# Kernel tuning notes

Measured on AMD Instinct MI355X. Metric: run time of the kernel, lower is better.

Reference implementation:

```python
import jax, jax.numpy as jnp
import numpy as np


def _perm_mats():
    E = np.zeros((36, 9), np.float32)
    D = np.zeros((9, 36), np.float32)
    c = 0
    for i in range(8):
        for j in range(i + 1, 9):
            E[c, i] = 1.0
            E[c, j] = 1.0
            D[i, c] = 1.0
            D[j, c] = 1.0
            c += 1
    assert c == 36
    return E, D


def setup_inputs() -> dict:
    key = jax.random.key(0)
    B = 32768
    # binary candidate mask: [B, 9 digits, 9 rows, 9 cols]
    mask = jnp.round(jax.random.uniform(key, (B, 9, 9, 9), dtype=jnp.float32))
    E, D = _perm_mats()
    return {"mask": mask, "enc": jnp.asarray(E), "dec": jnp.asarray(D)}


def _nn_compare(x, v):
    # NNCompare: triangular bump == 1 exactly when x == v (for integer-valued x)
    return jnp.minimum(jax.nn.relu(x - (v - 1.0)), jax.nn.relu((v + 1.0) - x))


def _nn_and(x, y):
    return jnp.clip(jnp.minimum(x, y), 0.0, 1.0)


def reference(mask, enc, dec):
    B = mask.shape[0]
    # encode_permutations: 1x1 conv 9 -> 36 (pair selection)
    perms = jnp.einsum('oc,bchw->bohw', enc, mask)          # [B,36,9,9]
    perms = _nn_compare(perms, 2.0)                          # cell contains exactly this pair
    # sum_all_permutations: 1x1 conv 36 -> 1, then == 1
    sum_p = _nn_compare(jnp.sum(perms, axis=1, keepdims=True), 1.0)  # [B,1,9,9]
    perms = _nn_and(perms, sum_p)                            # broadcast over 36 channels
    # box downsample: grouped 3x3 stride-3 sum conv
    down = perms.reshape(B, 36, 3, 3, 3, 3).sum(axis=(3, 5))  # [B,36,3,3]
    down = _nn_compare(down, 2.0)                              # exactly two such cells in box
    up = jnp.repeat(jnp.repeat(down, 3, axis=2), 3, axis=3)    # [B,36,9,9]
    up = _nn_and(up, 1.0 - perms)                              # other cells in the box
    # decode_permutations: 1x1 conv 36 -> 9
    erase = jnp.einsum('oc,bchw->bohw', dec, up)               # [B,9,9,9]
    return _nn_and(mask, 1.0 - erase)
```

## Files before the change

### kernel.cpp

```cpp
#include <hip/hip_runtime.h>
#include <stdint.h>


#define NB 16
#define ELEMS (NB * 729)
#define NWORDS (ELEMS / 4)
#define NBOX (NB * 9)

__global__ __launch_bounds__(256) void sudoku_naked_pair_kernel(
    const float* __restrict__ mask, float* __restrict__ out) {
  __shared__ uint32_t lds32[NWORDS];
  uint8_t* lds8 = (uint8_t*)lds32;

  const int tid = threadIdx.x;
  const size_t base = (size_t)blockIdx.x * ELEMS;

  const float4* in4 = (const float4*)(mask + base);
  for (int i = tid; i < NWORDS; i += 256) {
    float4 v = in4[i];
    lds32[i] = (uint32_t)(v.x != 0.0f)
             | ((uint32_t)(v.y != 0.0f) << 8)
             | ((uint32_t)(v.z != 0.0f) << 16)
             | ((uint32_t)(v.w != 0.0f) << 24);
  }
  __syncthreads();

  if (tid < NBOX) {
    const int b = tid / 9, bi = tid - b * 9;
    const int boxbase = b * 729 + (bi / 3) * 27 + (bi % 3) * 3;

    uint32_t cellm[9] = {0, 0, 0, 0, 0, 0, 0, 0, 0};
#pragma unroll
    for (int d = 0; d < 9; ++d) {
      const uint8_t* p = lds8 + boxbase + d * 81;
#pragma unroll
      for (int r = 0; r < 3; ++r)
#pragma unroll
        for (int c = 0; c < 3; ++c)
          cellm[r * 3 + c] |= ((uint32_t)p[r * 9 + c] & 1u) << d;
    }

    uint32_t pairm[9];
#pragma unroll
    for (int j = 0; j < 9; ++j)
      pairm[j] = (__popc(cellm[j]) == 2) ? cellm[j] : 0u;

    bool naked[9];
#pragma unroll
    for (int j = 0; j < 9; ++j) {
      int cnt = 0;
#pragma unroll
      for (int k = 0; k < 9; ++k) cnt += (pairm[k] == pairm[j]);
      naked[j] = (pairm[j] != 0u) && (cnt == 2);
    }

#pragma unroll
    for (int j = 0; j < 9; ++j) {
      uint32_t er = 0;
#pragma unroll
      for (int k = 0; k < 9; ++k)
        if (naked[k] && pairm[k] != pairm[j]) er |= pairm[k];
      cellm[j] &= ~er;
    }

#pragma unroll
    for (int d = 0; d < 9; ++d) {
      uint8_t* p = lds8 + boxbase + d * 81;
#pragma unroll
      for (int r = 0; r < 3; ++r)
#pragma unroll
        for (int c = 0; c < 3; ++c)
          p[r * 9 + c] = (uint8_t)((cellm[r * 3 + c] >> d) & 1u);
    }
  }
  __syncthreads();

  float4* out4 = (float4*)(out + base);
  for (int i = tid; i < NWORDS; i += 256) {
    uint32_t w = lds32[i];
    float4 v;
    v.x = (float)(w & 0xFFu);
    v.y = (float)((w >> 8) & 0xFFu);
    v.z = (float)((w >> 16) & 0xFFu);
    v.w = (float)(w >> 24);
    out4[i] = v;
  }
}

extern "C" void kernel_launch(void* const* d_in, const int* in_sizes, int n_in,
                              void* d_out, int out_size, void* d_ws, size_t ws_size,
                              hipStream_t stream) {
  const float* mask = (const float*)d_in[0];
  float* out = (float*)d_out;
  const int B = in_sizes[0] / 729;
  const int grid = B / NB;
  sudoku_naked_pair_kernel<<<grid, 256, 0, stream>>>(mask, out);
}
```

Measured before the change: 183.5 us.

## Replace LDS-staged block kernel with one-thread-per-box direct global access

Removes the shared-memory staging and the two barriers. Each thread now loads its box's 81 candidate floats straight from global memory, computes naked-pair eliminations in registers, and writes results directly. This aims to raise occupancy and remove idle threads and LDS traffic. In exchange, global accesses become small strided scalar reads and writes that coalesce poorly, and register pressure rises.

```diff
diff --git a/kernel.cpp b/kernel.cpp
--- a/kernel.cpp
+++ b/kernel.cpp
@@ -2,89 +2,64 @@
 #include <stdint.h>
 
 
-#define NB 16
-#define ELEMS (NB * 729)
-#define NWORDS (ELEMS / 4)
-#define NBOX (NB * 9)
+__global__ __launch_bounds__(256) void sudoku_box_kernel(
+    const float* __restrict__ mask, float* __restrict__ out) {
+  const int t = blockIdx.x * 256 + threadIdx.x;
+  const int board = t / 9;
+  const int bi = t - board * 9;
+  const int base = board * 729 + (bi / 3) * 27 + (bi % 3) * 3;
 
-__global__ __launch_bounds__(256) void sudoku_naked_pair_kernel(
-    const float* __restrict__ mask, float* __restrict__ out) {
-  __shared__ uint32_t lds32[NWORDS];
-  uint8_t* lds8 = (uint8_t*)lds32;
+  const float* p = mask + base;
+  float v[9][3][3];
+#pragma unroll
+  for (int d = 0; d < 9; ++d)
+#pragma unroll
+    for (int r = 0; r < 3; ++r)
+#pragma unroll
+      for (int c = 0; c < 3; ++c)
+        v[d][r][c] = p[d * 81 + r * 9 + c];
 
-  const int tid = threadIdx.x;
-  const size_t base = (size_t)blockIdx.x * ELEMS;
+  uint32_t cellm[9] = {0, 0, 0, 0, 0, 0, 0, 0, 0};
+#pragma unroll
+  for (int d = 0; d < 9; ++d)
+#pragma unroll
+    for (int r = 0; r < 3; ++r)
+#pragma unroll
+      for (int c = 0; c < 3; ++c)
+        cellm[r * 3 + c] |= (v[d][r][c] != 0.0f ? 1u : 0u) << d;
 
-  const float4* in4 = (const float4*)(mask + base);
-  for (int i = tid; i < NWORDS; i += 256) {
-    float4 v = in4[i];
-    lds32[i] = (uint32_t)(v.x != 0.0f)
-             | ((uint32_t)(v.y != 0.0f) << 8)
-             | ((uint32_t)(v.z != 0.0f) << 16)
-             | ((uint32_t)(v.w != 0.0f) << 24);
+  uint32_t pairm[9];
+#pragma unroll
+  for (int j = 0; j < 9; ++j)
+    pairm[j] = (__popc(cellm[j]) == 2) ? cellm[j] : 0u;
+
+  bool naked[9];
+#pragma unroll
+  for (int j = 0; j < 9; ++j) {
+    int cnt = 0;
+#pragma unroll
+    for (int k = 0; k < 9; ++k) cnt += (pairm[k] == pairm[j]);
+    naked[j] = (pairm[j] != 0u) && (cnt == 2);
   }
-  __syncthreads();
 
-  if (tid < NBOX) {
-    const int b = tid / 9, bi = tid - b * 9;
-    const int boxbase = b * 729 + (bi / 3) * 27 + (bi % 3) * 3;
+  uint32_t fin[9];
+#pragma unroll
+  for (int j = 0; j < 9; ++j) {
+    uint32_t er = 0;
+#pragma unroll
+    for (int k = 0; k < 9; ++k)
+      if (naked[k] && pairm[k] != pairm[j]) er |= pairm[k];
+    fin[j] = cellm[j] & ~er;
+  }
 
-    uint32_t cellm[9] = {0, 0, 0, 0, 0, 0, 0, 0, 0};
+  float* q = out + base;
 #pragma unroll
-    for (int d = 0; d < 9; ++d) {
-      const uint8_t* p = lds8 + boxbase + d * 81;
+  for (int d = 0; d < 9; ++d)
 #pragma unroll
-      for (int r = 0; r < 3; ++r)
+    for (int r = 0; r < 3; ++r)
 #pragma unroll
-        for (int c = 0; c < 3; ++c)
-          cellm[r * 3 + c] |= ((uint32_t)p[r * 9 + c] & 1u) << d;
-    }
-
-    uint32_t pairm[9];
-#pragma unroll
-    for (int j = 0; j < 9; ++j)
-      pairm[j] = (__popc(cellm[j]) == 2) ? cellm[j] : 0u;
-
-    bool naked[9];
-#pragma unroll
-    for (int j = 0; j < 9; ++j) {
-      int cnt = 0;
-#pragma unroll
-      for (int k = 0; k < 9; ++k) cnt += (pairm[k] == pairm[j]);
-      naked[j] = (pairm[j] != 0u) && (cnt == 2);
-    }
-
-#pragma unroll
-    for (int j = 0; j < 9; ++j) {
-      uint32_t er = 0;
-#pragma unroll
-      for (int k = 0; k < 9; ++k)
-        if (naked[k] && pairm[k] != pairm[j]) er |= pairm[k];
-      cellm[j] &= ~er;
-    }
-
-#pragma unroll
-    for (int d = 0; d < 9; ++d) {
-      uint8_t* p = lds8 + boxbase + d * 81;
-#pragma unroll
-      for (int r = 0; r < 3; ++r)
-#pragma unroll
-        for (int c = 0; c < 3; ++c)
-          p[r * 9 + c] = (uint8_t)((cellm[r * 3 + c] >> d) & 1u);
-    }
-  }
-  __syncthreads();
-
-  float4* out4 = (float4*)(out + base);
-  for (int i = tid; i < NWORDS; i += 256) {
-    uint32_t w = lds32[i];
-    float4 v;
-    v.x = (float)(w & 0xFFu);
-    v.y = (float)((w >> 8) & 0xFFu);
-    v.z = (float)((w >> 16) & 0xFFu);
-    v.w = (float)(w >> 24);
-    out4[i] = v;
-  }
+      for (int c = 0; c < 3; ++c)
+        q[d * 81 + r * 9 + c] = (float)((fin[r * 3 + c] >> d) & 1u);
 }
 
 extern "C" void kernel_launch(void* const* d_in, const int* in_sizes, int n_in,
@@ -93,6 +68,7 @@
   const float* mask = (const float*)d_in[0];
   float* out = (float*)d_out;
   const int B = in_sizes[0] / 729;
-  const int grid = B / NB;
-  sudoku_naked_pair_kernel<<<grid, 256, 0, stream>>>(mask, out);
+  const int nbox = B * 9;
+  const int grid = nbox / 256;
+  sudoku_box_kernel<<<grid, 256, 0, stream>>>(mask, out);
 }
```

Result: faster. 179.7 us (-2.1%).
